# Optimization experiments

Measured on AMD Instinct MI355X. Metric: run time of the kernel, lower is better.

The kernel has to match this reference:

```python
import jax, jax.numpy as jnp
import numpy as np

B, S, D, E, H, K = 4, 2048, 1024, 8, 4096, 2


def setup_inputs() -> dict:
    key = jax.random.key(0)
    ks = jax.random.split(key, 6)
    scale_in = 0.02  # keep logits/activations in a sane range
    return {
        "x": jax.random.normal(ks[0], (B, S, D), jnp.float32),
        "gate_w": jax.random.normal(ks[1], (D, E), jnp.float32) * scale_in,
        "noise_weight": jnp.zeros((E,), jnp.float32),  # torch init: zeros
        "noise": jax.random.normal(ks[2], (B, S, E), jnp.float32),
        "w1": jax.random.normal(ks[3], (E, D, H), jnp.float32) * scale_in,
        "b1": jnp.zeros((E, H), jnp.float32),
        "w2": jax.random.normal(ks[4], (E, D, H), jnp.float32) * scale_in,
        "b2": jnp.zeros((E, H), jnp.float32),
        "wp": jax.random.normal(ks[5], (E, H, D), jnp.float32) * scale_in,
        "bp": jnp.zeros((E, D), jnp.float32),
    }


def _moe(x, gate_w, noise_weight, noise, w1, b1, w2, b2, wp, bp):
    b, s, d = x.shape
    # --- noisy top-k gate ---
    logits = jnp.einsum("bsd,de->bse", x, gate_w)          # [B,S,E]
    logits_noisy = logits + noise * noise_weight            # noisy_std = 1.0
    top_v, top_i = jax.lax.top_k(logits_noisy, K)           # [B,S,K]
    # softmax over sparse logits (-inf elsewhere) == softmax over the top-k values
    probs_k = jax.nn.softmax(top_v, axis=-1)                # [B,S,K]
    onehot = jax.nn.one_hot(top_i, E, dtype=x.dtype)        # [B,S,K,E]
    gated = jnp.einsum("bsk,bske->bse", probs_k, onehot)    # [B,S,E]

    # --- dispatch / expert SwiGLU / weighted combine ---
    xf = x.reshape(b * s, d)                                # [T,D]
    gf = gated.reshape(b * s, E).T                          # [E,T]

    def body(acc, p):
        w1e, b1e, w2e, b2e, wpe, bpe, ge = p
        h = (xf @ w1e + b1e) * jax.nn.silu(xf @ w2e + b2e)  # [T,H] SwiGLU
        out = h @ wpe + bpe                                 # [T,D]
        return acc + ge[:, None] * out, None

    acc, _ = jax.lax.scan(body, jnp.zeros_like(xf), (w1, b1, w2, b2, wp, bp, gf))
    return acc.reshape(b, s, d)


def reference(x, gate_w, noise_weight, noise, w1, b1, w2, b2, wp, bp):
    return _moe(x, gate_w, noise_weight, noise, w1, b1, w2, b2, wp, bp)
```

## Files before the change

kernel.cpp:

```cpp
#include <hip/hip_runtime.h>


#define T_TOK 8192
#define DDIM 1024
#define EEXP 8
#define HDIM 4096
#define RMAX 17408

typedef short short8 __attribute__((ext_vector_type(8)));
typedef float f32x4 __attribute__((ext_vector_type(4)));
typedef unsigned short ushort4v __attribute__((ext_vector_type(4)));
typedef unsigned int u32;

__device__ __forceinline__ unsigned short f2bf(float f) {
  unsigned u = __builtin_bit_cast(unsigned, f);
  return (unsigned short)((u + 0x7FFFu + ((u >> 16) & 1u)) >> 16);
}
__device__ __forceinline__ void gl_lds16(const void* g, void* l) {
  __builtin_amdgcn_global_load_lds((const u32 __attribute__((address_space(1)))*)g,
                                   (u32 __attribute__((address_space(3)))*)l, 16, 0, 0);
}
#define MFMA_BF16 __builtin_amdgcn_mfma_f32_16x16x32_bf16

__global__ void k_init(int* __restrict__ rowtok, float* __restrict__ rowp,
                       int* __restrict__ counts, int* __restrict__ cursor,
                       float4* __restrict__ out4) {
  int i = blockIdx.x * 256 + threadIdx.x;
  if (i < RMAX) { rowtok[i] = 0; rowp[i] = 0.f; }
  if (i < EEXP) { counts[i] = 0; cursor[i] = 0; }
  float4 z = {0.f, 0.f, 0.f, 0.f};
  out4[i] = z;
  out4[i + 1048576] = z;
}

__global__ void k_convert_all(const float* __restrict__ w1, const float* __restrict__ w2,
                              const float* __restrict__ wp,
                              unsigned short* __restrict__ w1s, unsigned short* __restrict__ w2s,
                              unsigned short* __restrict__ wps) {
  __shared__ float lbuf[64 * 129];
  int bid = blockIdx.x;
  int seg = bid >> 12;
  int t = bid & 4095;
  const float* src; unsigned short* dst; int N, K, ct, kt, e;
  e = t >> 9;
  if (seg == 0)      { src = w1; dst = w1s; N = HDIM; K = DDIM; ct = (t >> 4) & 31; kt = t & 15; }
  else if (seg == 1) { src = w2; dst = w2s; N = HDIM; K = DDIM; ct = (t >> 4) & 31; kt = t & 15; }
  else               { src = wp; dst = wps; N = DDIM; K = HDIM; ct = (t >> 6) & 7;  kt = t & 63; }
  int tid = threadIdx.x;
  const float* s = src + (size_t)e * K * N + (size_t)(kt * 64) * N + ct * 128;
#pragma unroll
  for (int q = 0; q < 8; q++) {
    int idx = q * 256 + tid;
    int row = idx >> 5, c4 = (idx & 31) * 4;
    float4 v = *(const float4*)(s + (size_t)row * N + c4);
    lbuf[row * 129 + c4 + 0] = v.x;
    lbuf[row * 129 + c4 + 1] = v.y;
    lbuf[row * 129 + c4 + 2] = v.z;
    lbuf[row * 129 + c4 + 3] = v.w;
  }
  __syncthreads();
  unsigned short* dt = dst + ((size_t)(e * (N / 128) + ct) * (K / 64) + kt) * 8192;
#pragma unroll
  for (int q = 0; q < 4; q++) {
    int idx = q * 256 + tid;
    int kc = idx & 7, n = idx >> 3;
    short8 o;
#pragma unroll
    for (int j = 0; j < 8; j++) o[j] = (short)f2bf(lbuf[(kc * 8 + j) * 129 + n]);
    int byte = (n * 128 + kc * 16) ^ ((n & 7) << 4);
    *(short8*)((char*)dt + byte) = o;
  }
}

__launch_bounds__(256)
__global__ void k_gate(const float* __restrict__ x, const float* __restrict__ gw,
                       const float* __restrict__ nwt, const float* __restrict__ noi,
                       int* __restrict__ tki, float* __restrict__ tkp,
                       int* __restrict__ counts, unsigned short* __restrict__ xb) {
  __shared__ float gwT[8][1024];
  int tid = threadIdx.x;
#pragma unroll
  for (int q = 0; q < 32; q++) {
    int flat = q * 256 + tid;
    gwT[flat & 7][flat >> 3] = gw[flat];
  }
  __syncthreads();
  int wave = tid >> 6, l = tid & 63;
  int t = blockIdx.x * 4 + wave;
  float acc[8] = {0.f, 0.f, 0.f, 0.f, 0.f, 0.f, 0.f, 0.f};
  const float4* xr = (const float4*)(x + (size_t)t * DDIM);
#pragma unroll
  for (int i = 0; i < 4; i++) {
    float4 xv = xr[l + i * 64];
    int d0 = (l + i * 64) * 4;
    ushort4v o;
    o.x = f2bf(xv.x); o.y = f2bf(xv.y); o.z = f2bf(xv.z); o.w = f2bf(xv.w);
    *(ushort4v*)(xb + (size_t)t * DDIM + d0) = o;
#pragma unroll
    for (int e = 0; e < 8; e++) {
      float4 gv = *(const float4*)&gwT[e][d0];
      acc[e] += xv.x * gv.x + xv.y * gv.y + xv.z * gv.z + xv.w * gv.w;
    }
  }
#pragma unroll
  for (int s = 1; s < 64; s <<= 1) {
#pragma unroll
    for (int e = 0; e < 8; e++) acc[e] += __shfl_xor(acc[e], s, 64);
  }
  if (l == 0) {
    float nl[8];
#pragma unroll
    for (int e = 0; e < 8; e++) nl[e] = acc[e] + noi[t * 8 + e] * nwt[e];
    int i0 = 0; float v0 = nl[0];
#pragma unroll
    for (int e = 1; e < 8; e++) if (nl[e] > v0) { v0 = nl[e]; i0 = e; }
    int i1 = -1; float v1 = -3.4e38f;
#pragma unroll
    for (int e = 0; e < 8; e++) if (e != i0 && nl[e] > v1) { v1 = nl[e]; i1 = e; }
    float ex = __expf(v1 - v0);
    float p0 = 1.f / (1.f + ex);
    float p1 = ex * p0;
    tki[2 * t] = i0; tki[2 * t + 1] = i1;
    tkp[2 * t] = p0; tkp[2 * t + 1] = p1;
    atomicAdd(&counts[i0], 1);
    atomicAdd(&counts[i1], 1);
  }
}

__global__ void k_prefix(const int* __restrict__ counts, int* __restrict__ basep) {
  if (threadIdx.x == 0) {
    int b = 0;
    for (int e = 0; e < EEXP; e++) { basep[e] = b; b += (counts[e] + 127) & ~127; }
  }
}

__global__ void k_scatter(const int* __restrict__ tki, const float* __restrict__ tkp,
                          const int* __restrict__ basep, int* __restrict__ cursor,
                          int* __restrict__ rowtok, float* __restrict__ rowp) {
  int t = blockIdx.x * 256 + threadIdx.x;
  if (t >= T_TOK) return;
#pragma unroll
  for (int k = 0; k < 2; k++) {
    int e = tki[2 * t + k];
    int pos = atomicAdd(&cursor[e], 1);
    int row = basep[e] + pos;
    rowtok[row] = t;
    rowp[row] = tkp[2 * t + k];
  }
}

__launch_bounds__(256, 2)
__global__ void k_gemm1(const unsigned short* __restrict__ xb,
                        const unsigned short* __restrict__ w1s, const unsigned short* __restrict__ w2s,
                        const float* __restrict__ b1g, const float* __restrict__ b2g,
                        const int* __restrict__ counts, const int* __restrict__ basep,
                        const int* __restrict__ rowtok,
                        unsigned short* __restrict__ hout) {
  int lin = blockIdx.x;
  int orig = (lin & 7) * 2048 + (lin >> 3);
  int ct = orig & 31;
  int yy = orig >> 5;
  int e = yy >> 6;
  int rt = yy & 63;
  int cnt = counts[e];
  if (rt >= ((cnt + 127) >> 7)) return;
  int row0 = basep[e] + rt * 128;
  int col0 = ct * 128;

  __shared__ char smem[49152];
  __shared__ int s_tok[128];
  __shared__ float s_b1[128], s_b2[128];

  int tid = threadIdx.x;
  if (tid < 128) {
    s_tok[tid] = rowtok[row0 + tid];
    s_b1[tid] = b1g[e * HDIM + col0 + tid];
    s_b2[tid] = b2g[e * HDIM + col0 + tid];
  }
  __syncthreads();

  int wave = tid >> 6, l = tid & 63;
  int wr = (wave >> 1) << 6, wc = (wave & 1) << 6;
  int g = l >> 4, ln = l & 15;

  int sr[4], stok[4], sxor[4];
#pragma unroll
  for (int q = 0; q < 4; q++) {
    int flat = q * 256 + tid;
    sr[q] = flat;
    int r = flat >> 3, c = flat & 7;
    stok[q] = s_tok[r];
    sxor[q] = (c ^ (r & 7)) << 3;
  }

  f32x4 zero = {0.f, 0.f, 0.f, 0.f};
  f32x4 acc_a[4][4], acc_b[4][4];
#pragma unroll
  for (int m = 0; m < 4; m++)
#pragma unroll
    for (int n = 0; n < 4; n++) { acc_a[m][n] = zero; acc_b[m][n] = zero; }

  const unsigned short* w1t = w1s + ((size_t)(e * 32 + ct) * 16) * 8192;
  const unsigned short* w2t = w2s + ((size_t)(e * 32 + ct) * 16) * 8192;

  for (int kt = 0; kt < 16; kt++) {
#pragma unroll
    for (int q = 0; q < 4; q++) {
      gl_lds16(xb + (size_t)stok[q] * DDIM + kt * 64 + sxor[q], smem + sr[q] * 16);
      gl_lds16(w1t + (size_t)kt * 8192 + sr[q] * 8, smem + 16384 + sr[q] * 16);
      gl_lds16(w2t + (size_t)kt * 8192 + sr[q] * 8, smem + 32768 + sr[q] * 16);
    }
    __syncthreads();
#pragma unroll
    for (int ks = 0; ks < 2; ks++) {
      int kb = ks * 64 + g * 16;
      short8 af[4], bf1[4], bf2[4];
#pragma unroll
      for (int m = 0; m < 4; m++) {
        int r = wr + m * 16 + ln;
        af[m] = *(const short8*)(smem + ((r * 128 + kb) ^ ((r & 7) << 4)));
      }
#pragma unroll
      for (int n = 0; n < 4; n++) {
        int r = wc + n * 16 + ln;
        int byte = (r * 128 + kb) ^ ((r & 7) << 4);
        bf1[n] = *(const short8*)(smem + 16384 + byte);
        bf2[n] = *(const short8*)(smem + 32768 + byte);
      }
#pragma unroll
      for (int m = 0; m < 4; m++)
#pragma unroll
        for (int n = 0; n < 4; n++) {
          acc_a[m][n] = MFMA_BF16(af[m], bf1[n], acc_a[m][n], 0, 0, 0);
          acc_b[m][n] = MFMA_BF16(af[m], bf2[n], acc_b[m][n], 0, 0, 0);
        }
    }
    __syncthreads();
  }
  unsigned short* ht = (unsigned short*)smem;
#pragma unroll
  for (int m = 0; m < 4; m++)
#pragma unroll
    for (int n = 0; n < 4; n++)
#pragma unroll
      for (int r = 0; r < 4; r++) {
        int row = wr + m * 16 + g * 4 + r;
        int col = wc + n * 16 + ln;
        float a = acc_a[m][n][r] + s_b1[col];
        float b = acc_b[m][n][r] + s_b2[col];
        float hv = a * (b / (1.f + __expf(-b)));
        ht[row * 128 + col] = f2bf(hv);
      }
  __syncthreads();
#pragma unroll
  for (int q = 0; q < 8; q++) {
    int idx = q * 256 + tid;
    int row = idx >> 4, chunk = idx & 15;
    short8 v = *(const short8*)(smem + idx * 16);
    *(short8*)(hout + (size_t)(row0 + row) * HDIM + col0 + chunk * 8) = v;
  }
}

__launch_bounds__(256, 2)
__global__ void k_gemm2(const unsigned short* __restrict__ hin,
                        const unsigned short* __restrict__ wps, const float* __restrict__ bpg,
                        const int* __restrict__ counts, const int* __restrict__ basep,
                        const int* __restrict__ rowtok, const float* __restrict__ rowp,
                        float* __restrict__ outp) {
  int lin = blockIdx.x;
  int orig = (lin & 7) * 512 + (lin >> 3);
  int ct = orig & 7;
  int yy = orig >> 3;
  int e = yy >> 6;
  int rt = yy & 63;
  int cnt = counts[e];
  if (rt >= ((cnt + 127) >> 7)) return;
  int row0 = basep[e] + rt * 128;
  int col0 = ct * 128;

  __shared__ char smem[32768];
  __shared__ int s_tok[128];
  __shared__ float s_p[128], s_bp[128];
  int tid = threadIdx.x;
  if (tid < 128) {
    s_tok[tid] = rowtok[row0 + tid];
    s_p[tid] = rowp[row0 + tid];
    s_bp[tid] = bpg[e * DDIM + col0 + tid];
  }
  __syncthreads();

  int wave = tid >> 6, l = tid & 63;
  int wr = (wave >> 1) << 6, wc = (wave & 1) << 6;
  int g = l >> 4, ln = l & 15;

  int sr[4], srow[4], sxor[4];
#pragma unroll
  for (int q = 0; q < 4; q++) {
    int flat = q * 256 + tid;
    sr[q] = flat;
    int r = flat >> 3, c = flat & 7;
    srow[q] = row0 + r;
    sxor[q] = (c ^ (r & 7)) << 3;
  }

  f32x4 zero = {0.f, 0.f, 0.f, 0.f};
  f32x4 acc[4][4];
#pragma unroll
  for (int m = 0; m < 4; m++)
#pragma unroll
    for (int n = 0; n < 4; n++) acc[m][n] = zero;

  const unsigned short* wpt = wps + ((size_t)(e * 8 + ct) * 64) * 8192;

  for (int kt = 0; kt < 64; kt++) {
#pragma unroll
    for (int q = 0; q < 4; q++) {
      gl_lds16(hin + (size_t)srow[q] * HDIM + kt * 64 + sxor[q], smem + sr[q] * 16);
      gl_lds16(wpt + (size_t)kt * 8192 + sr[q] * 8, smem + 16384 + sr[q] * 16);
    }
    __syncthreads();
#pragma unroll
    for (int ks = 0; ks < 2; ks++) {
      int kb = ks * 64 + g * 16;
      short8 af[4], bf[4];
#pragma unroll
      for (int m = 0; m < 4; m++) {
        int r = wr + m * 16 + ln;
        af[m] = *(const short8*)(smem + ((r * 128 + kb) ^ ((r & 7) << 4)));
      }
#pragma unroll
      for (int n = 0; n < 4; n++) {
        int r = wc + n * 16 + ln;
        bf[n] = *(const short8*)(smem + 16384 + ((r * 128 + kb) ^ ((r & 7) << 4)));
      }
#pragma unroll
      for (int m = 0; m < 4; m++)
#pragma unroll
        for (int n = 0; n < 4; n++)
          acc[m][n] = MFMA_BF16(af[m], bf[n], acc[m][n], 0, 0, 0);
    }
    __syncthreads();
  }

#pragma unroll
  for (int m = 0; m < 4; m++)
#pragma unroll
    for (int r = 0; r < 4; r++) {
      int row = wr + m * 16 + g * 4 + r;
      float p = s_p[row];
      if (p != 0.f) {
        size_t obase = (size_t)s_tok[row] * DDIM + col0;
#pragma unroll
        for (int n = 0; n < 4; n++) {
          int col = wc + n * 16 + ln;
          atomicAdd(&outp[obase + col], p * (acc[m][n][r] + s_bp[col]));
        }
      }
    }
}

extern "C" void kernel_launch(void* const* d_in, const int* in_sizes, int n_in,
                              void* d_out, int out_size, void* d_ws, size_t ws_size,
                              hipStream_t stream) {
  const float* x   = (const float*)d_in[0];
  const float* gw  = (const float*)d_in[1];
  const float* nwt = (const float*)d_in[2];
  const float* noi = (const float*)d_in[3];
  const float* w1  = (const float*)d_in[4];
  const float* b1  = (const float*)d_in[5];
  const float* w2  = (const float*)d_in[6];
  const float* b2  = (const float*)d_in[7];
  const float* wp  = (const float*)d_in[8];
  const float* bp  = (const float*)d_in[9];
  float* outp = (float*)d_out;
  char* ws = (char*)d_ws;

  constexpr size_t SZ_W = (size_t)EEXP * DDIM * HDIM * 2;
  constexpr size_t OFF_XB  = 0;
  constexpr size_t OFF_W1S = OFF_XB + (size_t)T_TOK * DDIM * 2;
  constexpr size_t OFF_W2S = OFF_W1S + SZ_W;
  constexpr size_t OFF_WPS = OFF_W2S + SZ_W;
  constexpr size_t OFF_H   = OFF_WPS + SZ_W;
  constexpr size_t OFF_RT  = OFF_H + (size_t)RMAX * HDIM * 2;
  constexpr size_t OFF_RP  = OFF_RT + (size_t)RMAX * 4;
  constexpr size_t OFF_TKI = OFF_RP + (size_t)RMAX * 4;
  constexpr size_t OFF_TKP = OFF_TKI + (size_t)T_TOK * 2 * 4;
  constexpr size_t OFF_CNT = OFF_TKP + (size_t)T_TOK * 2 * 4;
  constexpr size_t OFF_BAS = OFF_CNT + 256;
  constexpr size_t OFF_CUR = OFF_BAS + 256;

  unsigned short* xb  = (unsigned short*)(ws + OFF_XB);
  unsigned short* w1s = (unsigned short*)(ws + OFF_W1S);
  unsigned short* w2s = (unsigned short*)(ws + OFF_W2S);
  unsigned short* wps = (unsigned short*)(ws + OFF_WPS);
  unsigned short* h   = (unsigned short*)(ws + OFF_H);
  int*   rowtok = (int*)(ws + OFF_RT);
  float* rowp   = (float*)(ws + OFF_RP);
  int*   tki    = (int*)(ws + OFF_TKI);
  float* tkp    = (float*)(ws + OFF_TKP);
  int*   counts = (int*)(ws + OFF_CNT);
  int*   basep  = (int*)(ws + OFF_BAS);
  int*   cursor = (int*)(ws + OFF_CUR);

  dim3 blk(256);
  k_init<<<dim3(4096), blk, 0, stream>>>(rowtok, rowp, counts, cursor, (float4*)outp);
  k_gate<<<dim3(T_TOK / 4), blk, 0, stream>>>(x, gw, nwt, noi, tki, tkp, counts, xb);
  k_convert_all<<<dim3(12288), blk, 0, stream>>>(w1, w2, wp, w1s, w2s, wps);
  k_prefix<<<dim3(1), dim3(64), 0, stream>>>(counts, basep);
  k_scatter<<<dim3(T_TOK / 256), blk, 0, stream>>>(tki, tkp, basep, cursor, rowtok, rowp);
  k_gemm1<<<dim3(16384), blk, 0, stream>>>(xb, w1s, w2s, b1, b2, counts, basep, rowtok, h);
  k_gemm2<<<dim3(4096), blk, 0, stream>>>(h, wps, bp, counts, basep, rowtok, rowp, outp);
  (void)in_sizes; (void)n_in; (void)out_size; (void)ws_size;
}
```

Measured before the change: 922.1 us.

## Rewrite gate/up GEMM as 256-row, 8-wave tile with double-buffered LDS pipeline

The first expert GEMM moves to 512-thread blocks computing 256x128 tiles for both W1 and W2. Operand staging is double-buffered in 128 KB of LDS with partial vmcnt waits, so loads for the next K slice overlap the MFMAs of the current one. The loop also raises wave priority around the MFMA bursts. Expert segments are now padded to 256 rows, which adds some padding work, and both GEMMs drop the swizzled 1D grid for a plain 2D grid, which may change L2 reuse of weights.

```diff
diff --git a/kernel.cpp b/kernel.cpp
--- a/kernel.cpp
+++ b/kernel.cpp
@@ -5,7 +5,7 @@
 #define DDIM 1024
 #define EEXP 8
 #define HDIM 4096
-#define RMAX 17408
+#define RMAX 18432
 
 typedef short short8 __attribute__((ext_vector_type(8)));
 typedef float f32x4 __attribute__((ext_vector_type(4)));
@@ -130,7 +130,7 @@
 __global__ void k_prefix(const int* __restrict__ counts, int* __restrict__ basep) {
   if (threadIdx.x == 0) {
     int b = 0;
-    for (int e = 0; e < EEXP; e++) { basep[e] = b; b += (counts[e] + 127) & ~127; }
+    for (int e = 0; e < EEXP; e++) { basep[e] = b; b += (counts[e] + 255) & ~255; }
   }
 }
 
@@ -149,115 +149,150 @@
   }
 }
 
-__launch_bounds__(256, 2)
+__launch_bounds__(512, 1)
 __global__ void k_gemm1(const unsigned short* __restrict__ xb,
                         const unsigned short* __restrict__ w1s, const unsigned short* __restrict__ w2s,
                         const float* __restrict__ b1g, const float* __restrict__ b2g,
                         const int* __restrict__ counts, const int* __restrict__ basep,
                         const int* __restrict__ rowtok,
                         unsigned short* __restrict__ hout) {
-  int lin = blockIdx.x;
-  int orig = (lin & 7) * 2048 + (lin >> 3);
-  int ct = orig & 31;
-  int yy = orig >> 5;
-  int e = yy >> 6;
-  int rt = yy & 63;
+  int e = blockIdx.y / 33;
+  int rt = blockIdx.y % 33;
   int cnt = counts[e];
-  if (rt >= ((cnt + 127) >> 7)) return;
-  int row0 = basep[e] + rt * 128;
+  if (rt >= ((cnt + 255) >> 8)) return;
+  int ct = blockIdx.x;
+  int row0 = basep[e] + rt * 256;
   int col0 = ct * 128;
 
-  __shared__ char smem[49152];
-  __shared__ int s_tok[128];
+  __shared__ char smem[131072];
+  __shared__ int s_tok[256];
   __shared__ float s_b1[128], s_b2[128];
 
   int tid = threadIdx.x;
+  if (tid < 256) s_tok[tid] = rowtok[row0 + tid];
   if (tid < 128) {
-    s_tok[tid] = rowtok[row0 + tid];
     s_b1[tid] = b1g[e * HDIM + col0 + tid];
     s_b2[tid] = b2g[e * HDIM + col0 + tid];
   }
   __syncthreads();
 
   int wave = tid >> 6, l = tid & 63;
-  int wr = (wave >> 1) << 6, wc = (wave & 1) << 6;
+  int wm = wave >> 2, wn = wave & 3;
   int g = l >> 4, ln = l & 15;
 
-  int sr[4], stok[4], sxor[4];
-#pragma unroll
-  for (int q = 0; q < 4; q++) {
-    int flat = q * 256 + tid;
-    sr[q] = flat;
-    int r = flat >> 3, c = flat & 7;
-    stok[q] = s_tok[r];
-    sxor[q] = (c ^ (r & 7)) << 3;
+  size_t a_src[2][2];
+#pragma unroll
+  for (int h = 0; h < 2; h++)
+#pragma unroll
+    for (int j = 0; j < 2; j++) {
+      int c = j * 512 + tid;
+      int r = c >> 3, cc = (c & 7) ^ (r & 7);
+      a_src[h][j] = (size_t)s_tok[h * 128 + r] * 2048 + (size_t)(cc * 16);
+    }
+
+  int a_off[4][2], b_off[2][2];
+#pragma unroll
+  for (int m = 0; m < 4; m++) {
+    int r = wm * 64 + m * 16 + ln;
+    a_off[m][0] = (r * 128 + g * 16) ^ ((r & 7) << 4);
+    a_off[m][1] = (r * 128 + 64 + g * 16) ^ ((r & 7) << 4);
+  }
+#pragma unroll
+  for (int n = 0; n < 2; n++) {
+    int r = wn * 32 + n * 16 + ln;
+    b_off[n][0] = (r * 128 + g * 16) ^ ((r & 7) << 4);
+    b_off[n][1] = (r * 128 + 64 + g * 16) ^ ((r & 7) << 4);
   }
 
   f32x4 zero = {0.f, 0.f, 0.f, 0.f};
-  f32x4 acc_a[4][4], acc_b[4][4];
-#pragma unroll
-  for (int m = 0; m < 4; m++)
-#pragma unroll
-    for (int n = 0; n < 4; n++) { acc_a[m][n] = zero; acc_b[m][n] = zero; }
-
-  const unsigned short* w1t = w1s + ((size_t)(e * 32 + ct) * 16) * 8192;
-  const unsigned short* w2t = w2s + ((size_t)(e * 32 + ct) * 16) * 8192;
-
-  for (int kt = 0; kt < 16; kt++) {
-#pragma unroll
-    for (int q = 0; q < 4; q++) {
-      gl_lds16(xb + (size_t)stok[q] * DDIM + kt * 64 + sxor[q], smem + sr[q] * 16);
-      gl_lds16(w1t + (size_t)kt * 8192 + sr[q] * 8, smem + 16384 + sr[q] * 16);
-      gl_lds16(w2t + (size_t)kt * 8192 + sr[q] * 8, smem + 32768 + sr[q] * 16);
-    }
-    __syncthreads();
-#pragma unroll
-    for (int ks = 0; ks < 2; ks++) {
-      int kb = ks * 64 + g * 16;
-      short8 af[4], bf1[4], bf2[4];
-#pragma unroll
-      for (int m = 0; m < 4; m++) {
-        int r = wr + m * 16 + ln;
-        af[m] = *(const short8*)(smem + ((r * 128 + kb) ^ ((r & 7) << 4)));
-      }
-#pragma unroll
-      for (int n = 0; n < 4; n++) {
-        int r = wc + n * 16 + ln;
-        int byte = (r * 128 + kb) ^ ((r & 7) << 4);
-        bf1[n] = *(const short8*)(smem + 16384 + byte);
-        bf2[n] = *(const short8*)(smem + 32768 + byte);
-      }
-#pragma unroll
-      for (int m = 0; m < 4; m++)
-#pragma unroll
-        for (int n = 0; n < 4; n++) {
-          acc_a[m][n] = MFMA_BF16(af[m], bf1[n], acc_a[m][n], 0, 0, 0);
-          acc_b[m][n] = MFMA_BF16(af[m], bf2[n], acc_b[m][n], 0, 0, 0);
+  f32x4 accA[2][4][2], accB[2][4][2];
+#pragma unroll
+  for (int h = 0; h < 2; h++)
+#pragma unroll
+    for (int m = 0; m < 4; m++)
+#pragma unroll
+      for (int n = 0; n < 2; n++) { accA[h][m][n] = zero; accB[h][m][n] = zero; }
+
+  const char* xbb = (const char*)xb;
+  const char* w1t = (const char*)w1s + (size_t)(e * 32 + ct) * 16 * 16384;
+  const char* w2t = (const char*)w2s + (size_t)(e * 32 + ct) * 16 * 16384;
+
+  short8 af[4][2], bf[2][2];
+
+#define ST_A(h, par, kt)                                                          \
+  gl_lds16(xbb + a_src[h][0] + (size_t)(kt) * 128, smem + ((par) * 2 + (h)) * 16384 + tid * 16);            \
+  gl_lds16(xbb + a_src[h][1] + (size_t)(kt) * 128, smem + ((par) * 2 + (h)) * 16384 + (512 + tid) * 16);
+#define ST_B(wt, b, par, kt)                                                      \
+  gl_lds16((wt) + (size_t)(kt) * 16384 + tid * 16, smem + 65536 + ((par) * 2 + (b)) * 16384 + tid * 16);    \
+  gl_lds16((wt) + (size_t)(kt) * 16384 + (512 + tid) * 16, smem + 65536 + ((par) * 2 + (b)) * 16384 + (512 + tid) * 16);
+
+#define PH(h, bslot, par, RA, STAGE_STMT, ACC) {                                  \
+    asm volatile("s_waitcnt vmcnt(8)" ::: "memory");                              \
+    __builtin_amdgcn_s_barrier();                                                 \
+    char* Ab = smem + ((par) * 2 + (h)) * 16384;                                  \
+    char* Bb = smem + 65536 + ((par) * 2 + (bslot)) * 16384;                      \
+    if (RA) {                                                                     \
+      _Pragma("unroll") for (int m = 0; m < 4; m++) {                             \
+        af[m][0] = *(const short8*)(Ab + a_off[m][0]);                            \
+        af[m][1] = *(const short8*)(Ab + a_off[m][1]);                            \
+      }                                                                           \
+    }                                                                             \
+    _Pragma("unroll") for (int n = 0; n < 2; n++) {                               \
+      bf[n][0] = *(const short8*)(Bb + b_off[n][0]);                              \
+      bf[n][1] = *(const short8*)(Bb + b_off[n][1]);                              \
+    }                                                                             \
+    STAGE_STMT;                                                                   \
+    __builtin_amdgcn_s_setprio(1);                                                \
+    _Pragma("unroll") for (int m = 0; m < 4; m++)                                 \
+      _Pragma("unroll") for (int n = 0; n < 2; n++) {                             \
+        ACC[h][m][n] = MFMA_BF16(af[m][0], bf[n][0], ACC[h][m][n], 0, 0, 0);      \
+        ACC[h][m][n] = MFMA_BF16(af[m][1], bf[n][1], ACC[h][m][n], 0, 0, 0);      \
+      }                                                                           \
+    __builtin_amdgcn_s_setprio(0);                                                \
+  }
+
+  ST_A(0, 0, 0) ST_B(w1t, 0, 0, 0) ST_B(w2t, 1, 0, 0) ST_A(1, 0, 0)
+  ST_A(0, 1, 1) ST_B(w1t, 0, 1, 1)
+
+  for (int i = 0; i < 8; i++) {
+    int kto = 2 * i + 1;
+    int kt2 = (2 * i + 2) & 15, kt3 = (2 * i + 3) & 15;
+    PH(0, 0, 0, 1, ST_B(w2t, 1, 1, kto), accA)
+    PH(0, 1, 0, 0, ST_A(1, 1, kto),      accB)
+    PH(1, 0, 0, 1, ST_A(0, 0, kt2),      accA)
+    PH(1, 1, 0, 0, ST_B(w1t, 0, 0, kt2), accB)
+    PH(0, 0, 1, 1, ST_B(w2t, 1, 0, kt2), accA)
+    PH(0, 1, 1, 0, ST_A(1, 0, kt2),      accB)
+    PH(1, 0, 1, 1, ST_A(0, 1, kt3),      accA)
+    PH(1, 1, 1, 0, ST_B(w1t, 0, 1, kt3), accB)
+  }
+
+  asm volatile("s_waitcnt vmcnt(0)" ::: "memory");
+  __syncthreads();
+
+  unsigned short* ht = (unsigned short*)smem;
+#pragma unroll
+  for (int h = 0; h < 2; h++)
+#pragma unroll
+    for (int m = 0; m < 4; m++)
+#pragma unroll
+      for (int n = 0; n < 2; n++)
+#pragma unroll
+        for (int r = 0; r < 4; r++) {
+          int row = h * 128 + wm * 64 + m * 16 + g * 4 + r;
+          int col = wn * 32 + n * 16 + ln;
+          float a = accA[h][m][n][r] + s_b1[col];
+          float b = accB[h][m][n][r] + s_b2[col];
+          float hv = a * (b / (1.f + __expf(-b)));
+          ht[row * 128 + col] = f2bf(hv);
         }
-    }
-    __syncthreads();
-  }
-  unsigned short* ht = (unsigned short*)smem;
-#pragma unroll
-  for (int m = 0; m < 4; m++)
-#pragma unroll
-    for (int n = 0; n < 4; n++)
-#pragma unroll
-      for (int r = 0; r < 4; r++) {
-        int row = wr + m * 16 + g * 4 + r;
-        int col = wc + n * 16 + ln;
-        float a = acc_a[m][n][r] + s_b1[col];
-        float b = acc_b[m][n][r] + s_b2[col];
-        float hv = a * (b / (1.f + __expf(-b)));
-        ht[row * 128 + col] = f2bf(hv);
-      }
   __syncthreads();
 #pragma unroll
   for (int q = 0; q < 8; q++) {
-    int idx = q * 256 + tid;
-    int row = idx >> 4, chunk = idx & 15;
+    int idx = q * 512 + tid;
+    int row = idx >> 4, cc = (idx & 15) * 8;
     short8 v = *(const short8*)(smem + idx * 16);
-    *(short8*)(hout + (size_t)(row0 + row) * HDIM + col0 + chunk * 8) = v;
+    *(short8*)(hout + (size_t)(row0 + row) * HDIM + col0 + cc) = v;
   }
 }
 
@@ -267,14 +302,11 @@
                         const int* __restrict__ counts, const int* __restrict__ basep,
                         const int* __restrict__ rowtok, const float* __restrict__ rowp,
                         float* __restrict__ outp) {
-  int lin = blockIdx.x;
-  int orig = (lin & 7) * 512 + (lin >> 3);
-  int ct = orig & 7;
-  int yy = orig >> 3;
-  int e = yy >> 6;
-  int rt = yy & 63;
+  int e = blockIdx.y >> 6;
+  int rt = blockIdx.y & 63;
   int cnt = counts[e];
   if (rt >= ((cnt + 127) >> 7)) return;
+  int ct = blockIdx.x;
   int row0 = basep[e] + rt * 128;
   int col0 = ct * 128;
 
@@ -322,7 +354,7 @@
 #pragma unroll
     for (int ks = 0; ks < 2; ks++) {
       int kb = ks * 64 + g * 16;
-      short8 af[4], bf[4];
+      short8 af[4], bfr[4];
 #pragma unroll
       for (int m = 0; m < 4; m++) {
         int r = wr + m * 16 + ln;
@@ -331,13 +363,13 @@
 #pragma unroll
       for (int n = 0; n < 4; n++) {
         int r = wc + n * 16 + ln;
-        bf[n] = *(const short8*)(smem + 16384 + ((r * 128 + kb) ^ ((r & 7) << 4)));
+        bfr[n] = *(const short8*)(smem + 16384 + ((r * 128 + kb) ^ ((r & 7) << 4)));
       }
 #pragma unroll
       for (int m = 0; m < 4; m++)
 #pragma unroll
         for (int n = 0; n < 4; n++)
-          acc[m][n] = MFMA_BF16(af[m], bf[n], acc[m][n], 0, 0, 0);
+          acc[m][n] = MFMA_BF16(af[m], bfr[n], acc[m][n], 0, 0, 0);
     }
     __syncthreads();
   }
@@ -408,7 +440,7 @@
   k_convert_all<<<dim3(12288), blk, 0, stream>>>(w1, w2, wp, w1s, w2s, wps);
   k_prefix<<<dim3(1), dim3(64), 0, stream>>>(counts, basep);
   k_scatter<<<dim3(T_TOK / 256), blk, 0, stream>>>(tki, tkp, basep, cursor, rowtok, rowp);
-  k_gemm1<<<dim3(16384), blk, 0, stream>>>(xb, w1s, w2s, b1, b2, counts, basep, rowtok, h);
-  k_gemm2<<<dim3(4096), blk, 0, stream>>>(h, wps, bp, counts, basep, rowtok, rowp, outp);
+  k_gemm1<<<dim3(HDIM / 128, EEXP * 33), dim3(512), 0, stream>>>(xb, w1s, w2s, b1, b2, counts, basep, rowtok, h);
+  k_gemm2<<<dim3(DDIM / 128, EEXP * 64), blk, 0, stream>>>(h, wps, bp, counts, basep, rowtok, rowp, outp);
   (void)in_sizes; (void)n_in; (void)out_size; (void)ws_size;
 }
```

Result: slower. 954.5 us (+3.5%).
